# Kernel optimization log

Hardware: AMD Instinct MI355X
Metric: run time of the kernel (lower is better)

## Reference

```python
import jax, jax.numpy as jnp
import numpy as np

N_USERS, N_ITEMS, D, K, B = 1000000, 500000, 64, 256, 16384


def _l2norm(x, axis=1, eps=1e-12):
    n = jnp.sqrt(jnp.sum(x * x, axis=axis, keepdims=True))
    return x / jnp.maximum(n, eps)


def _sinkhorn(out):
    # out: [B, K]; 3 Sinkhorn-Knopp iterations on Q = exp(out/0.05).T
    Q = jnp.exp(out / 0.05).T            # [K, B]
    Kd, Bd = Q.shape
    Q = Q / jnp.sum(Q)
    for _ in range(3):
        Q = Q / (jnp.sum(Q, axis=1, keepdims=True) * Kd)
        Q = Q / (jnp.sum(Q, axis=0, keepdims=True) * Bd)
    return (Q * Bd).T                    # [B, K]


def _ce(q, code, gamma):
    return -jnp.mean(jnp.sum(q * jax.nn.log_softmax(code / gamma, axis=1), axis=1))


def setup_inputs() -> dict:
    key = jax.random.key(0)
    ks = jax.random.split(key, 8)
    return {
        "user_embeddings": jax.random.normal(ks[0], (N_USERS, D), jnp.float32),
        "id_embeddings": jax.random.normal(ks[1], (N_ITEMS, D), jnp.float32),
        "image_embeddings": jax.random.normal(ks[2], (N_ITEMS, D), jnp.float32),
        "text_embeddings": jax.random.normal(ks[3], (N_ITEMS, D), jnp.float32),
        "users": jax.random.randint(ks[4], (B,), 0, N_USERS, jnp.int32),
        "items": jax.random.randint(ks[5], (B,), 0, N_ITEMS, jnp.int32),
        "feat2code_w": jax.random.normal(ks[6], (K, D), jnp.float32),
        "ii2code_w": jax.random.normal(ks[7], (K, D), jnp.float32),
        "gamma": jnp.asarray(0.5, jnp.float32),
    }


def reference(user_embeddings, id_embeddings, image_embeddings, text_embeddings,
              users, items, feat2code_w, ii2code_w, gamma):
    # in-place clamp / weight renorm in torch happen under no_grad: value changes,
    # gradient wrt the parameter is identity -> straight-through here.
    g = gamma + jax.lax.stop_gradient(jnp.clip(gamma, 0.01, 0.99) - gamma)
    w_feat = feat2code_w + jax.lax.stop_gradient(_l2norm(feat2code_w) - feat2code_w)
    w_ii = ii2code_w + jax.lax.stop_gradient(_l2norm(ii2code_w) - ii2code_w)

    u = _l2norm(user_embeddings[users])     # [B, D]
    i_id = _l2norm(id_embeddings[items])
    i_im = _l2norm(image_embeddings[items])
    i_tx = _l2norm(text_embeddings[items])

    code_user = u @ w_feat.T                # [B, K]
    code_id = i_id @ w_feat.T
    code_id_ii = i_id @ w_ii.T
    code_image_ii = i_im @ w_ii.T
    code_text_ii = i_tx @ w_ii.T

    q_id = jax.lax.stop_gradient(_sinkhorn(code_id))
    q_user = jax.lax.stop_gradient(_sinkhorn(code_user))
    q_id_ii = jax.lax.stop_gradient(_sinkhorn(code_id_ii))
    q_image_ii = jax.lax.stop_gradient(_sinkhorn(code_image_ii))
    q_text_ii = jax.lax.stop_gradient(_sinkhorn(code_text_ii))

    loss = _ce(q_user, code_id, g) + _ce(q_id, code_user, g)
    align = (_ce(q_id_ii, code_image_ii, g) + _ce(q_id_ii, code_text_ii, g)
             + _ce(q_image_ii, code_id_ii, g) + _ce(q_image_ii, code_text_ii, g)
             + _ce(q_text_ii, code_id_ii, g) + _ce(q_text_ii, code_image_ii, g))
    return loss / 2 + align / 6
```

## Files before the change

kernel.cpp:

```cpp
#include <hip/hip_runtime.h>
#include <hip/hip_bf16.h>
#include <math.h>

#define BATCH 16384
#define DIM   64
#define KCODE 256

typedef unsigned short ushort_t;
typedef __attribute__((ext_vector_type(8))) short bf16x8;
typedef __attribute__((ext_vector_type(4))) float f32x4;

#define MFMA16 __builtin_amdgcn_mfma_f32_16x16x32_bf16

static __device__ __forceinline__ float ss4(float4 a) {
    return a.x*a.x + a.y*a.y + a.z*a.z + a.w*a.w;
}
static __device__ __forceinline__ short f2bs(float f) {
    unsigned u = __float_as_uint(f);
    u += 0x7FFFu + ((u >> 16) & 1u);
    return (short)(u >> 16);
}
static __device__ __forceinline__ bf16x8 pack8(float4 a, float4 b, float s) {
    bf16x8 r;
    r[0]=f2bs(a.x*s); r[1]=f2bs(a.y*s); r[2]=f2bs(a.z*s); r[3]=f2bs(a.w*s);
    r[4]=f2bs(b.x*s); r[5]=f2bs(b.y*s); r[6]=f2bs(b.z*s); r[7]=f2bs(b.w*s);
    return r;
}

__global__ __launch_bounds__(256) void k1_prep_gemm_cs1(
    const float* __restrict__ ue, const float* __restrict__ ie,
    const float* __restrict__ me, const float* __restrict__ te,
    const int* __restrict__ users, const int* __restrict__ items,
    const float* __restrict__ wfeat, const float* __restrict__ wii,
    ushort_t* __restrict__ An, ushort_t* __restrict__ Wn,
    float* __restrict__ cs1)
{
    const int m  = blockIdx.y;
    const int bx = blockIdx.x;
    const int t  = threadIdx.x;
    const int aset = (m==0) ? 0 : (m<3) ? 1 : (m==3) ? 2 : 3;
    const int wset = (m<2) ? 0 : 1;
    const float* asrc = (aset==0)?ue:(aset==1)?ie:(aset==2)?me:te;
    const int*  idxv = (m==0)?users:items;
    const float* wsrc = (wset==0)?wfeat:wii;
    const bool store_w = ((m==0 || m==2) && bx==0);
    const bool store_a = (m != 2);

    __shared__ short Wl[16384];
    __shared__ short Al[4096];
    __shared__ float redA[4][64];
    __shared__ float csl[256];

    {
        const float4* wp = (const float4*)(wsrc + t*DIM);
        float4 q[16]; float ss = 0.f;
        #pragma unroll
        for (int i=0;i<16;++i){ q[i]=wp[i]; ss += ss4(q[i]); }
        const float inv = 1.0f / fmaxf(sqrtf(ss), 1e-12f);
        const int kt = t>>4, lr = t&15;
        #pragma unroll
        for (int kk=0;kk<2;++kk)
            #pragma unroll
            for (int fs=0;fs<4;++fs){
                const int qi = kk*8 + fs*2;
                bf16x8 pk = pack8(q[qi], q[qi+1], inv);
                const int cid = (kt*2+kk)*64 + fs*16 + lr;
                *(bf16x8*)&Wl[cid*8] = pk;
                if (store_w)
                    *(bf16x8*)(Wn + ((size_t)wset*KCODE + t)*DIM + kk*32 + fs*8) = pk;
            }
    }

    const int rb = t&63, seg = t>>6;
    const int gidx = idxv[bx*64 + rb];
    const float4* ap = (const float4*)(asrc + (size_t)gidx*DIM + seg*16);
    float4 a0=ap[0], a1=ap[1], a2=ap[2], a3=ap[3];
    redA[seg][rb] = ss4(a0)+ss4(a1)+ss4(a2)+ss4(a3);
    csl[t] = 0.f;
    __syncthreads();

    {
        const float tot = redA[0][rb]+redA[1][rb]+redA[2][rb]+redA[3][rb];
        const float inv = 1.0f/fmaxf(sqrtf(tot),1e-12f);
        bf16x8 c0 = pack8(a0, a1, inv);
        bf16x8 c1 = pack8(a2, a3, inv);
        const int kk = seg>>1, fs0 = (seg&1)*2;
        const int base = ((rb>>4)*2 + kk)*64;
        *(bf16x8*)&Al[(base + fs0*16     + (rb&15))*8] = c0;
        *(bf16x8*)&Al[(base + (fs0+1)*16 + (rb&15))*8] = c1;
        if (store_a) {
            ushort_t* dst = An + ((size_t)aset*BATCH + bx*64 + rb)*DIM + seg*16;
            *(bf16x8*)dst       = c0;
            *(bf16x8*)(dst + 8) = c1;
        }
    }
    __syncthreads();

    const int w = t>>6, lane = t&63;
    bf16x8 af0 = *(bf16x8*)&Al[((w*2+0)*64 + lane)*8];
    bf16x8 af1 = *(bf16x8*)&Al[((w*2+1)*64 + lane)*8];
    #pragma unroll 4
    for (int kt=0; kt<16; ++kt){
        bf16x8 wf0 = *(bf16x8*)&Wl[((kt*2+0)*64 + lane)*8];
        bf16x8 wf1 = *(bf16x8*)&Wl[((kt*2+1)*64 + lane)*8];
        f32x4 acc = {0.f,0.f,0.f,0.f};
        acc = MFMA16(af0, wf0, acc, 0,0,0);
        acc = MFMA16(af1, wf1, acc, 0,0,0);
        float es = __expf(20.f*acc[0]) + __expf(20.f*acc[1])
                 + __expf(20.f*acc[2]) + __expf(20.f*acc[3]);
        atomicAdd(&csl[kt*16 + (lane&15)], es);
    }
    __syncthreads();
    atomicAdd(&cs1[m*KCODE + t], csl[t]);
}

__global__ __launch_bounds__(256) void k_pass(
    const ushort_t* __restrict__ An, const ushort_t* __restrict__ Wn,
    const float* __restrict__ cs_prev, float* __restrict__ cs_next)
{
    const int m = blockIdx.y;
    const int aset = (m==0)?0:(m<3)?1:(m==3)?2:3;
    const int wset = (m<2)?0:1;
    const int t = threadIdx.x, lane = t&63, w = t>>6;

    __shared__ short Wl[16384];
    __shared__ float csl[256];

    #pragma unroll
    for (int c8=0;c8<8;++c8){
        const int cid = c8*256 + t;
        const int kt = cid>>7, kk=(cid>>6)&1, ln=cid&63;
        const ushort_t* src = Wn + ((size_t)wset*KCODE + kt*16 + (ln&15))*DIM
                                 + kk*32 + (ln>>4)*8;
        *(bf16x8*)&Wl[cid*8] = *(const bf16x8*)src;
    }
    csl[t] = 0.f;
    float ar[16];
    #pragma unroll
    for (int kt=0;kt<16;++kt)
        ar[kt] = __builtin_amdgcn_rcpf(256.0f * cs_prev[m*KCODE + kt*16 + (lane&15)]);
    __syncthreads();

    float csp[16];
    #pragma unroll
    for (int kt=0;kt<16;++kt) csp[kt]=0.f;

    for (int rt = blockIdx.x*4 + w; rt < BATCH/16; rt += gridDim.x*4){
        const int r0 = rt*16;
        const ushort_t* ab = An + ((size_t)aset*BATCH + r0 + (lane&15))*DIM + (lane>>4)*8;
        bf16x8 af0 = *(const bf16x8*)ab;
        bf16x8 af1 = *(const bf16x8*)(ab + 32);
        float ev[16][4];
        float sp0=0.f, sp1=0.f, sp2=0.f, sp3=0.f;
        #pragma unroll
        for (int kt=0;kt<16;++kt){
            bf16x8 wf0 = *(bf16x8*)&Wl[((kt*2+0)*64+lane)*8];
            bf16x8 wf1 = *(bf16x8*)&Wl[((kt*2+1)*64+lane)*8];
            f32x4 acc = {0.f,0.f,0.f,0.f};
            acc = MFMA16(af0, wf0, acc, 0,0,0);
            acc = MFMA16(af1, wf1, acc, 0,0,0);
            ev[kt][0]=__expf(20.f*acc[0]); ev[kt][1]=__expf(20.f*acc[1]);
            ev[kt][2]=__expf(20.f*acc[2]); ev[kt][3]=__expf(20.f*acc[3]);
            sp0 = fmaf(ar[kt], ev[kt][0], sp0);
            sp1 = fmaf(ar[kt], ev[kt][1], sp1);
            sp2 = fmaf(ar[kt], ev[kt][2], sp2);
            sp3 = fmaf(ar[kt], ev[kt][3], sp3);
        }
        #pragma unroll
        for (int off=8; off>=1; off>>=1){
            sp0 += __shfl_xor(sp0, off, 64);
            sp1 += __shfl_xor(sp1, off, 64);
            sp2 += __shfl_xor(sp2, off, 64);
            sp3 += __shfl_xor(sp3, off, 64);
        }
        const float b0 = __builtin_amdgcn_rcpf(16384.f*sp0);
        const float b1 = __builtin_amdgcn_rcpf(16384.f*sp1);
        const float b2 = __builtin_amdgcn_rcpf(16384.f*sp2);
        const float b3 = __builtin_amdgcn_rcpf(16384.f*sp3);
        #pragma unroll
        for (int kt=0;kt<16;++kt)
            csp[kt] += ev[kt][0]*b0 + ev[kt][1]*b1 + ev[kt][2]*b2 + ev[kt][3]*b3;
    }
    #pragma unroll
    for (int kt=0;kt<16;++kt)
        atomicAdd(&csl[kt*16 + (lane&15)], csp[kt]);
    __syncthreads();
    atomicAdd(&cs_next[m*KCODE + t], csl[t]);
}

__global__ __launch_bounds__(256) void k_ce(
    const ushort_t* __restrict__ An, const ushort_t* __restrict__ Wn,
    const float* __restrict__ cs3, const float* __restrict__ gamma_p,
    float* __restrict__ out)
{
    const int t = threadIdx.x, lane = t&63, w = t>>6;
    __shared__ short Wl[32768];
    __shared__ float al[1280];

    #pragma unroll
    for (int c16=0;c16<16;++c16){
        const int cid = c16*256 + t;
        const int ws = cid>>11, rem = cid&2047;
        const int kt = rem>>7, kk=(rem>>6)&1, ln=rem&63;
        const ushort_t* src = Wn + ((size_t)ws*KCODE + kt*16 + (ln&15))*DIM
                                 + kk*32 + (ln>>4)*8;
        *(bf16x8*)&Wl[cid*8] = *(const bf16x8*)src;
    }
    #pragma unroll
    for (int mm=0;mm<5;++mm)
        al[mm*256+t] = __builtin_amdgcn_rcpf(256.0f * cs3[mm*KCODE + t]);
    const float g = fminf(fmaxf(gamma_p[0], 0.01f), 0.99f);
    const float invg = 1.0f/g;
    __syncthreads();

    float wacc = 0.f;
    for (int rt = blockIdx.x*4 + w; rt < BATCH/16; rt += gridDim.x*4){
        const int r0 = rt*16;
        bf16x8 af[4][2];
        #pragma unroll
        for (int s=0;s<4;++s){
            const ushort_t* ab = An + ((size_t)s*BATCH + r0 + (lane&15))*DIM + (lane>>4)*8;
            af[s][0] = *(const bf16x8*)ab;
            af[s][1] = *(const bf16x8*)(ab + 32);
        }
        float S[5][4], L[5][4], DP[5][4];
        #pragma unroll
        for (int mm=0;mm<5;++mm)
            #pragma unroll
            for (int r=0;r<4;++r){ S[mm][r]=0.f; L[mm][r]=0.f; DP[mm][r]=0.f; }

        #pragma unroll 2
        for (int kt=0;kt<16;++kt){
            bf16x8 wf[2][2];
            #pragma unroll
            for (int ws=0;ws<2;++ws){
                wf[ws][0] = *(bf16x8*)&Wl[((ws*2048) + (kt*2+0)*64 + lane)*8];
                wf[ws][1] = *(bf16x8*)&Wl[((ws*2048) + (kt*2+1)*64 + lane)*8];
            }
            const f32x4 Z = {0.f,0.f,0.f,0.f};
            f32x4 c[5];
            c[0] = MFMA16(af[0][0], wf[0][0], Z, 0,0,0);
            c[0] = MFMA16(af[0][1], wf[0][1], c[0], 0,0,0);
            c[1] = MFMA16(af[1][0], wf[0][0], Z, 0,0,0);
            c[1] = MFMA16(af[1][1], wf[0][1], c[1], 0,0,0);
            c[2] = MFMA16(af[1][0], wf[1][0], Z, 0,0,0);
            c[2] = MFMA16(af[1][1], wf[1][1], c[2], 0,0,0);
            c[3] = MFMA16(af[2][0], wf[1][0], Z, 0,0,0);
            c[3] = MFMA16(af[2][1], wf[1][1], c[3], 0,0,0);
            c[4] = MFMA16(af[3][0], wf[1][0], Z, 0,0,0);
            c[4] = MFMA16(af[3][1], wf[1][1], c[4], 0,0,0);

            float am[5];
            #pragma unroll
            for (int mm=0;mm<5;++mm) am[mm] = al[mm*256 + kt*16 + (lane&15)];

            float fm[5][4];
            #pragma unroll
            for (int mm=0;mm<5;++mm)
                #pragma unroll
                for (int r=0;r<4;++r){
                    const float cv = c[mm][r];
                    const float f = am[mm] * __expf(20.f*cv);
                    fm[mm][r] = f;
                    S[mm][r] += f;
                    L[mm][r] += __expf(invg*cv);
                }
            #pragma unroll
            for (int r=0;r<4;++r){
                DP[0][r] = fmaf(fm[0][r], c[1][r], DP[0][r]);
                DP[1][r] = fmaf(fm[1][r], c[0][r], DP[1][r]);
                const float c34 = c[3][r]+c[4][r];
                const float c24 = c[2][r]+c[4][r];
                const float c23 = c[2][r]+c[3][r];
                DP[2][r] = fmaf(fm[2][r], c34, DP[2][r]);
                DP[3][r] = fmaf(fm[3][r], c24, DP[3][r]);
                DP[4][r] = fmaf(fm[4][r], c23, DP[4][r]);
            }
        }
        #pragma unroll
        for (int off=8; off>=1; off>>=1)
            #pragma unroll
            for (int mm=0;mm<5;++mm)
                #pragma unroll
                for (int r=0;r<4;++r){
                    S[mm][r]  += __shfl_xor(S[mm][r],  off, 64);
                    L[mm][r]  += __shfl_xor(L[mm][r],  off, 64);
                    DP[mm][r] += __shfl_xor(DP[mm][r], off, 64);
                }
        #pragma unroll
        for (int r=0;r<4;++r){
            const float u =
                0.5f*(DP[0][r]*__builtin_amdgcn_rcpf(S[0][r])
                    + DP[1][r]*__builtin_amdgcn_rcpf(S[1][r]))
              + (1.f/6.f)*(DP[2][r]*__builtin_amdgcn_rcpf(S[2][r])
                         + DP[3][r]*__builtin_amdgcn_rcpf(S[3][r])
                         + DP[4][r]*__builtin_amdgcn_rcpf(S[4][r]));
            const float Lr =
                0.5f*(__logf(L[0][r]) + __logf(L[1][r]))
              + (1.f/3.f)*(__logf(L[2][r]) + __logf(L[3][r]) + __logf(L[4][r]));
            wacc += Lr - invg*u;
        }
    }
    wacc += __shfl_xor(wacc, 16, 64);
    wacc += __shfl_xor(wacc, 32, 64);
    if (lane == 0) atomicAdd(out, wacc * (1.0f/16384.0f));
}

extern "C" void kernel_launch(void* const* d_in, const int* in_sizes, int n_in,
                              void* d_out, int out_size, void* d_ws, size_t ws_size,
                              hipStream_t stream)
{
    const float* ue    = (const float*)d_in[0];
    const float* ie    = (const float*)d_in[1];
    const float* me    = (const float*)d_in[2];
    const float* te    = (const float*)d_in[3];
    const int*   users = (const int*)d_in[4];
    const int*   items = (const int*)d_in[5];
    const float* wfeat = (const float*)d_in[6];
    const float* wii   = (const float*)d_in[7];
    const float* gamma = (const float*)d_in[8];
    float* out = (float*)d_out;

    ushort_t* An = (ushort_t*)d_ws;
    ushort_t* Wn = An + (size_t)4*BATCH*DIM;
    float* cs  = (float*)(Wn + 2*KCODE*DIM);
    float* cs1 = cs;
    float* cs2 = cs + 1280;
    float* cs3 = cs + 2560;

    hipMemsetAsync(out, 0, sizeof(float), stream);
    hipMemsetAsync(cs, 0, 3*1280*sizeof(float), stream);

    k1_prep_gemm_cs1<<<dim3(256,5), 256, 0, stream>>>(
        ue, ie, me, te, users, items, wfeat, wii, An, Wn, cs1);
    k_pass<<<dim3(128,5), 256, 0, stream>>>(An, Wn, cs1, cs2);
    k_pass<<<dim3(128,5), 256, 0, stream>>>(An, Wn, cs2, cs3);
    k_ce<<<256, 256, 0, stream>>>(An, Wn, cs3, gamma, out);
}
```

Measured before the change: 146.6 us.

## Merge prep, Sinkhorn passes and CE into one cooperative persistent kernel

Replaces the four separate launches and two memsets with a single cooperative kernel. It uses grid-wide syncs between the normalization/bf16 packing stage, the three Sinkhorn column-sum passes and the cross-entropy stage. The goal is to remove launch gaps and memset overhead, and to load both normalized weight sets into LDS once per block for all stages. In exchange the first Sinkhorn pass no longer runs in the prep stage, so it re-reads An from global memory. Each tile now also does per-tile shared atomics, and the grid size is capped by occupancy (74KB LDS per block).

```diff
diff --git a/kernel.cpp b/kernel.cpp
--- a/kernel.cpp
+++ b/kernel.cpp
@@ -1,6 +1,8 @@
 #include <hip/hip_runtime.h>
-#include <hip/hip_bf16.h>
+#include <hip/hip_cooperative_groups.h>
 #include <math.h>
+
+namespace cg = cooperative_groups;
 
 #define BATCH 16384
 #define DIM   64
@@ -27,194 +29,183 @@
     return r;
 }
 
-__global__ __launch_bounds__(256) void k1_prep_gemm_cs1(
+template<bool FIRST>
+static __device__ __forceinline__ void sink_pass(
+    const ushort_t* __restrict__ An, const short* __restrict__ Wl,
+    const float* __restrict__ al, float* __restrict__ csl,
+    int wid, int lane, int nW)
+{
+    for (int u = wid; u < 5120; u += nW) {
+        const int m = u >> 10, rt = u & 1023;
+        const int aset = (m==0) ? 0 : (m<3) ? 1 : (m==3) ? 2 : 3;
+        const int wset = (m<2) ? 0 : 1;
+        const ushort_t* ab = An + ((size_t)aset*BATCH + rt*16 + (lane&15))*DIM + (lane>>4)*8;
+        bf16x8 af0 = *(const bf16x8*)ab;
+        bf16x8 af1 = *(const bf16x8*)(ab + 32);
+        float csp[16];
+        if (FIRST) {
+            #pragma unroll
+            for (int kt=0;kt<16;++kt){
+                bf16x8 wf0 = *(const bf16x8*)&Wl[((wset*2048)+(kt*2+0)*64+lane)*8];
+                bf16x8 wf1 = *(const bf16x8*)&Wl[((wset*2048)+(kt*2+1)*64+lane)*8];
+                f32x4 acc = {0.f,0.f,0.f,0.f};
+                acc = MFMA16(af0, wf0, acc, 0,0,0);
+                acc = MFMA16(af1, wf1, acc, 0,0,0);
+                csp[kt] = __expf(20.f*acc[0]) + __expf(20.f*acc[1])
+                        + __expf(20.f*acc[2]) + __expf(20.f*acc[3]);
+            }
+        } else {
+            float ev[16][4];
+            float sp0=0.f, sp1=0.f, sp2=0.f, sp3=0.f;
+            #pragma unroll
+            for (int kt=0;kt<16;++kt){
+                bf16x8 wf0 = *(const bf16x8*)&Wl[((wset*2048)+(kt*2+0)*64+lane)*8];
+                bf16x8 wf1 = *(const bf16x8*)&Wl[((wset*2048)+(kt*2+1)*64+lane)*8];
+                f32x4 acc = {0.f,0.f,0.f,0.f};
+                acc = MFMA16(af0, wf0, acc, 0,0,0);
+                acc = MFMA16(af1, wf1, acc, 0,0,0);
+                ev[kt][0]=__expf(20.f*acc[0]); ev[kt][1]=__expf(20.f*acc[1]);
+                ev[kt][2]=__expf(20.f*acc[2]); ev[kt][3]=__expf(20.f*acc[3]);
+                const float a = al[m*KCODE + kt*16 + (lane&15)];
+                sp0 = fmaf(a, ev[kt][0], sp0);
+                sp1 = fmaf(a, ev[kt][1], sp1);
+                sp2 = fmaf(a, ev[kt][2], sp2);
+                sp3 = fmaf(a, ev[kt][3], sp3);
+            }
+            #pragma unroll
+            for (int off=8; off>=1; off>>=1){
+                sp0 += __shfl_xor(sp0, off, 64);
+                sp1 += __shfl_xor(sp1, off, 64);
+                sp2 += __shfl_xor(sp2, off, 64);
+                sp3 += __shfl_xor(sp3, off, 64);
+            }
+            const float b0 = __builtin_amdgcn_rcpf(16384.f*sp0);
+            const float b1 = __builtin_amdgcn_rcpf(16384.f*sp1);
+            const float b2 = __builtin_amdgcn_rcpf(16384.f*sp2);
+            const float b3 = __builtin_amdgcn_rcpf(16384.f*sp3);
+            #pragma unroll
+            for (int kt=0;kt<16;++kt)
+                csp[kt] = ev[kt][0]*b0 + ev[kt][1]*b1 + ev[kt][2]*b2 + ev[kt][3]*b3;
+        }
+        #pragma unroll
+        for (int kt=0;kt<16;++kt){
+            float v = csp[kt];
+            v += __shfl_xor(v, 16, 64);
+            v += __shfl_xor(v, 32, 64);
+            if (lane < 16) atomicAdd(&csl[m*KCODE + kt*16 + lane], v);
+        }
+    }
+}
+
+__global__ __launch_bounds__(256, 2) void cla_mega(
     const float* __restrict__ ue, const float* __restrict__ ie,
     const float* __restrict__ me, const float* __restrict__ te,
     const int* __restrict__ users, const int* __restrict__ items,
     const float* __restrict__ wfeat, const float* __restrict__ wii,
     ushort_t* __restrict__ An, ushort_t* __restrict__ Wn,
-    float* __restrict__ cs1)
-{
-    const int m  = blockIdx.y;
-    const int bx = blockIdx.x;
-    const int t  = threadIdx.x;
-    const int aset = (m==0) ? 0 : (m<3) ? 1 : (m==3) ? 2 : 3;
-    const int wset = (m<2) ? 0 : 1;
-    const float* asrc = (aset==0)?ue:(aset==1)?ie:(aset==2)?me:te;
-    const int*  idxv = (m==0)?users:items;
-    const float* wsrc = (wset==0)?wfeat:wii;
-    const bool store_w = ((m==0 || m==2) && bx==0);
-    const bool store_a = (m != 2);
-
-    __shared__ short Wl[16384];
-    __shared__ short Al[4096];
-    __shared__ float redA[4][64];
-    __shared__ float csl[256];
-
-    {
-        const float4* wp = (const float4*)(wsrc + t*DIM);
-        float4 q[16]; float ss = 0.f;
-        #pragma unroll
-        for (int i=0;i<16;++i){ q[i]=wp[i]; ss += ss4(q[i]); }
-        const float inv = 1.0f / fmaxf(sqrtf(ss), 1e-12f);
-        const int kt = t>>4, lr = t&15;
-        #pragma unroll
-        for (int kk=0;kk<2;++kk)
-            #pragma unroll
-            for (int fs=0;fs<4;++fs){
-                const int qi = kk*8 + fs*2;
-                bf16x8 pk = pack8(q[qi], q[qi+1], inv);
-                const int cid = (kt*2+kk)*64 + fs*16 + lr;
-                *(bf16x8*)&Wl[cid*8] = pk;
-                if (store_w)
-                    *(bf16x8*)(Wn + ((size_t)wset*KCODE + t)*DIM + kk*32 + fs*8) = pk;
-            }
-    }
-
-    const int rb = t&63, seg = t>>6;
-    const int gidx = idxv[bx*64 + rb];
-    const float4* ap = (const float4*)(asrc + (size_t)gidx*DIM + seg*16);
-    float4 a0=ap[0], a1=ap[1], a2=ap[2], a3=ap[3];
-    redA[seg][rb] = ss4(a0)+ss4(a1)+ss4(a2)+ss4(a3);
-    csl[t] = 0.f;
-    __syncthreads();
-
-    {
-        const float tot = redA[0][rb]+redA[1][rb]+redA[2][rb]+redA[3][rb];
-        const float inv = 1.0f/fmaxf(sqrtf(tot),1e-12f);
-        bf16x8 c0 = pack8(a0, a1, inv);
-        bf16x8 c1 = pack8(a2, a3, inv);
-        const int kk = seg>>1, fs0 = (seg&1)*2;
-        const int base = ((rb>>4)*2 + kk)*64;
-        *(bf16x8*)&Al[(base + fs0*16     + (rb&15))*8] = c0;
-        *(bf16x8*)&Al[(base + (fs0+1)*16 + (rb&15))*8] = c1;
-        if (store_a) {
-            ushort_t* dst = An + ((size_t)aset*BATCH + bx*64 + rb)*DIM + seg*16;
-            *(bf16x8*)dst       = c0;
-            *(bf16x8*)(dst + 8) = c1;
-        }
-    }
-    __syncthreads();
-
-    const int w = t>>6, lane = t&63;
-    bf16x8 af0 = *(bf16x8*)&Al[((w*2+0)*64 + lane)*8];
-    bf16x8 af1 = *(bf16x8*)&Al[((w*2+1)*64 + lane)*8];
-    #pragma unroll 4
-    for (int kt=0; kt<16; ++kt){
-        bf16x8 wf0 = *(bf16x8*)&Wl[((kt*2+0)*64 + lane)*8];
-        bf16x8 wf1 = *(bf16x8*)&Wl[((kt*2+1)*64 + lane)*8];
-        f32x4 acc = {0.f,0.f,0.f,0.f};
-        acc = MFMA16(af0, wf0, acc, 0,0,0);
-        acc = MFMA16(af1, wf1, acc, 0,0,0);
-        float es = __expf(20.f*acc[0]) + __expf(20.f*acc[1])
-                 + __expf(20.f*acc[2]) + __expf(20.f*acc[3]);
-        atomicAdd(&csl[kt*16 + (lane&15)], es);
-    }
-    __syncthreads();
-    atomicAdd(&cs1[m*KCODE + t], csl[t]);
-}
-
-__global__ __launch_bounds__(256) void k_pass(
-    const ushort_t* __restrict__ An, const ushort_t* __restrict__ Wn,
-    const float* __restrict__ cs_prev, float* __restrict__ cs_next)
-{
-    const int m = blockIdx.y;
-    const int aset = (m==0)?0:(m<3)?1:(m==3)?2:3;
-    const int wset = (m<2)?0:1;
-    const int t = threadIdx.x, lane = t&63, w = t>>6;
-
-    __shared__ short Wl[16384];
-    __shared__ float csl[256];
-
-    #pragma unroll
-    for (int c8=0;c8<8;++c8){
-        const int cid = c8*256 + t;
-        const int kt = cid>>7, kk=(cid>>6)&1, ln=cid&63;
-        const ushort_t* src = Wn + ((size_t)wset*KCODE + kt*16 + (ln&15))*DIM
-                                 + kk*32 + (ln>>4)*8;
-        *(bf16x8*)&Wl[cid*8] = *(const bf16x8*)src;
-    }
-    csl[t] = 0.f;
-    float ar[16];
-    #pragma unroll
-    for (int kt=0;kt<16;++kt)
-        ar[kt] = __builtin_amdgcn_rcpf(256.0f * cs_prev[m*KCODE + kt*16 + (lane&15)]);
-    __syncthreads();
-
-    float csp[16];
-    #pragma unroll
-    for (int kt=0;kt<16;++kt) csp[kt]=0.f;
-
-    for (int rt = blockIdx.x*4 + w; rt < BATCH/16; rt += gridDim.x*4){
-        const int r0 = rt*16;
-        const ushort_t* ab = An + ((size_t)aset*BATCH + r0 + (lane&15))*DIM + (lane>>4)*8;
-        bf16x8 af0 = *(const bf16x8*)ab;
-        bf16x8 af1 = *(const bf16x8*)(ab + 32);
-        float ev[16][4];
-        float sp0=0.f, sp1=0.f, sp2=0.f, sp3=0.f;
-        #pragma unroll
-        for (int kt=0;kt<16;++kt){
-            bf16x8 wf0 = *(bf16x8*)&Wl[((kt*2+0)*64+lane)*8];
-            bf16x8 wf1 = *(bf16x8*)&Wl[((kt*2+1)*64+lane)*8];
-            f32x4 acc = {0.f,0.f,0.f,0.f};
-            acc = MFMA16(af0, wf0, acc, 0,0,0);
-            acc = MFMA16(af1, wf1, acc, 0,0,0);
-            ev[kt][0]=__expf(20.f*acc[0]); ev[kt][1]=__expf(20.f*acc[1]);
-            ev[kt][2]=__expf(20.f*acc[2]); ev[kt][3]=__expf(20.f*acc[3]);
-            sp0 = fmaf(ar[kt], ev[kt][0], sp0);
-            sp1 = fmaf(ar[kt], ev[kt][1], sp1);
-            sp2 = fmaf(ar[kt], ev[kt][2], sp2);
-            sp3 = fmaf(ar[kt], ev[kt][3], sp3);
-        }
-        #pragma unroll
-        for (int off=8; off>=1; off>>=1){
-            sp0 += __shfl_xor(sp0, off, 64);
-            sp1 += __shfl_xor(sp1, off, 64);
-            sp2 += __shfl_xor(sp2, off, 64);
-            sp3 += __shfl_xor(sp3, off, 64);
-        }
-        const float b0 = __builtin_amdgcn_rcpf(16384.f*sp0);
-        const float b1 = __builtin_amdgcn_rcpf(16384.f*sp1);
-        const float b2 = __builtin_amdgcn_rcpf(16384.f*sp2);
-        const float b3 = __builtin_amdgcn_rcpf(16384.f*sp3);
-        #pragma unroll
-        for (int kt=0;kt<16;++kt)
-            csp[kt] += ev[kt][0]*b0 + ev[kt][1]*b1 + ev[kt][2]*b2 + ev[kt][3]*b3;
-    }
-    #pragma unroll
-    for (int kt=0;kt<16;++kt)
-        atomicAdd(&csl[kt*16 + (lane&15)], csp[kt]);
-    __syncthreads();
-    atomicAdd(&cs_next[m*KCODE + t], csl[t]);
-}
-
-__global__ __launch_bounds__(256) void k_ce(
-    const ushort_t* __restrict__ An, const ushort_t* __restrict__ Wn,
-    const float* __restrict__ cs3, const float* __restrict__ gamma_p,
+    float* __restrict__ cs, const float* __restrict__ gamma_p,
     float* __restrict__ out)
 {
-    const int t = threadIdx.x, lane = t&63, w = t>>6;
+    cg::grid_group gg = cg::this_grid();
+    const int t = threadIdx.x, lane = t & 63;
+    const int g = blockIdx.x*256 + t;
+    const int wid = (blockIdx.x*256 + t) >> 6;
+    const int nT = gridDim.x << 8;
+    const int nW = gridDim.x << 2;
+
     __shared__ short Wl[32768];
     __shared__ float al[1280];
-
-    #pragma unroll
-    for (int c16=0;c16<16;++c16){
-        const int cid = c16*256 + t;
-        const int ws = cid>>11, rem = cid&2047;
-        const int kt = rem>>7, kk=(rem>>6)&1, ln=rem&63;
-        const ushort_t* src = Wn + ((size_t)ws*KCODE + kt*16 + (ln&15))*DIM
-                                 + kk*32 + (ln>>4)*8;
-        *(bf16x8*)&Wl[cid*8] = *(const bf16x8*)src;
-    }
-    #pragma unroll
-    for (int mm=0;mm<5;++mm)
-        al[mm*256+t] = __builtin_amdgcn_rcpf(256.0f * cs3[mm*KCODE + t]);
-    const float g = fminf(fmaxf(gamma_p[0], 0.01f), 0.99f);
-    const float invg = 1.0f/g;
-    __syncthreads();
-
+    __shared__ float csl[1280];
+
+    for (int i = g; i < 3840; i += nT) cs[i] = 0.f;
+    if (g == 0) out[0] = 0.f;
+
+    for (int h = g; h < 2*4*BATCH; h += nT) {
+        const int row = h >> 1, half = h & 1;
+        const int set = row >> 14, r = row & (BATCH-1);
+        const float* src; int idx;
+        if (set == 0)      { src = ue; idx = users[r]; }
+        else if (set == 1) { src = ie; idx = items[r]; }
+        else if (set == 2) { src = me; idx = items[r]; }
+        else               { src = te; idx = items[r]; }
+        const float4* p = (const float4*)(src + (size_t)idx*DIM + half*32);
+        float4 q[8]; float ss = 0.f;
+        #pragma unroll
+        for (int i2=0;i2<8;++i2){ q[i2]=p[i2]; ss += ss4(q[i2]); }
+        ss += __shfl_xor(ss, 1, 64);
+        const float inv = 1.0f / fmaxf(sqrtf(ss), 1e-12f);
+        ushort_t* dst = An + ((size_t)set*BATCH + r)*DIM + half*32;
+        #pragma unroll
+        for (int j=0;j<4;++j)
+            *(bf16x8*)(dst + j*8) = pack8(q[2*j], q[2*j+1], inv);
+    }
+    for (int h = g; h < 2*2*KCODE; h += nT) {
+        const int wrow = h >> 1, half = h & 1;
+        const int wset = wrow >> 8, wr = wrow & 255;
+        const float* src = (wset ? wii : wfeat) + (size_t)wr*DIM + half*32;
+        const float4* p = (const float4*)src;
+        float4 q[8]; float ss = 0.f;
+        #pragma unroll
+        for (int i2=0;i2<8;++i2){ q[i2]=p[i2]; ss += ss4(q[i2]); }
+        ss += __shfl_xor(ss, 1, 64);
+        const float inv = 1.0f / fmaxf(sqrtf(ss), 1e-12f);
+        ushort_t* dst = Wn + ((size_t)wset*KCODE + wr)*DIM + half*32;
+        #pragma unroll
+        for (int j=0;j<4;++j)
+            *(bf16x8*)(dst + j*8) = pack8(q[2*j], q[2*j+1], inv);
+    }
+    gg.sync();
+
+    for (int cid = t; cid < 4096; cid += 256) {
+        const int ws2 = cid >> 11, rem = cid & 2047;
+        const int kt = rem >> 7, kk = (rem >> 6) & 1, ln = rem & 63;
+        const ushort_t* s2 = Wn + ((size_t)ws2*KCODE + kt*16 + (ln&15))*DIM
+                                + kk*32 + (ln>>4)*8;
+        *(bf16x8*)&Wl[cid*8] = *(const bf16x8*)s2;
+    }
+    #pragma unroll
+    for (int j=0;j<5;++j) csl[j*256+t] = 0.f;
+    __syncthreads();
+
+    sink_pass<true>(An, Wl, al, csl, wid, lane, nW);
+    __syncthreads();
+    #pragma unroll
+    for (int j=0;j<5;++j) atomicAdd(&cs[j*256+t], csl[j*256+t]);
+    gg.sync();
+
+    #pragma unroll
+    for (int j=0;j<5;++j){
+        al[j*256+t]  = __builtin_amdgcn_rcpf(256.0f * cs[j*256+t]);
+        csl[j*256+t] = 0.f;
+    }
+    __syncthreads();
+    sink_pass<false>(An, Wl, al, csl, wid, lane, nW);
+    __syncthreads();
+    #pragma unroll
+    for (int j=0;j<5;++j) atomicAdd(&cs[1280 + j*256+t], csl[j*256+t]);
+    gg.sync();
+
+    #pragma unroll
+    for (int j=0;j<5;++j){
+        al[j*256+t]  = __builtin_amdgcn_rcpf(256.0f * cs[1280 + j*256+t]);
+        csl[j*256+t] = 0.f;
+    }
+    __syncthreads();
+    sink_pass<false>(An, Wl, al, csl, wid, lane, nW);
+    __syncthreads();
+    #pragma unroll
+    for (int j=0;j<5;++j) atomicAdd(&cs[2560 + j*256+t], csl[j*256+t]);
+    gg.sync();
+
+    #pragma unroll
+    for (int j=0;j<5;++j)
+        al[j*256+t] = __builtin_amdgcn_rcpf(256.0f * cs[2560 + j*256+t]);
+    __syncthreads();
+
+    const float gam = fminf(fmaxf(gamma_p[0], 0.01f), 0.99f);
+    const float invg = 1.0f / gam;
     float wacc = 0.f;
-    for (int rt = blockIdx.x*4 + w; rt < BATCH/16; rt += gridDim.x*4){
+    for (int rt = wid; rt < 1024; rt += nW) {
         const int r0 = rt*16;
         bf16x8 af[4][2];
         #pragma unroll
@@ -233,9 +224,9 @@
         for (int kt=0;kt<16;++kt){
             bf16x8 wf[2][2];
             #pragma unroll
-            for (int ws=0;ws<2;++ws){
-                wf[ws][0] = *(bf16x8*)&Wl[((ws*2048) + (kt*2+0)*64 + lane)*8];
-                wf[ws][1] = *(bf16x8*)&Wl[((ws*2048) + (kt*2+1)*64 + lane)*8];
+            for (int ws2=0;ws2<2;++ws2){
+                wf[ws2][0] = *(const bf16x8*)&Wl[((ws2*2048)+(kt*2+0)*64+lane)*8];
+                wf[ws2][1] = *(const bf16x8*)&Wl[((ws2*2048)+(kt*2+1)*64+lane)*8];
             }
             const f32x4 Z = {0.f,0.f,0.f,0.f};
             f32x4 c[5];
@@ -252,7 +243,7 @@
 
             float am[5];
             #pragma unroll
-            for (int mm=0;mm<5;++mm) am[mm] = al[mm*256 + kt*16 + (lane&15)];
+            for (int mm=0;mm<5;++mm) am[mm] = al[mm*KCODE + kt*16 + (lane&15)];
 
             float fm[5][4];
             #pragma unroll
@@ -323,17 +314,16 @@
 
     ushort_t* An = (ushort_t*)d_ws;
     ushort_t* Wn = An + (size_t)4*BATCH*DIM;
-    float* cs  = (float*)(Wn + 2*KCODE*DIM);
-    float* cs1 = cs;
-    float* cs2 = cs + 1280;
-    float* cs3 = cs + 2560;
-
-    hipMemsetAsync(out, 0, sizeof(float), stream);
-    hipMemsetAsync(cs, 0, 3*1280*sizeof(float), stream);
-
-    k1_prep_gemm_cs1<<<dim3(256,5), 256, 0, stream>>>(
-        ue, ie, me, te, users, items, wfeat, wii, An, Wn, cs1);
-    k_pass<<<dim3(128,5), 256, 0, stream>>>(An, Wn, cs1, cs2);
-    k_pass<<<dim3(128,5), 256, 0, stream>>>(An, Wn, cs2, cs3);
-    k_ce<<<256, 256, 0, stream>>>(An, Wn, cs3, gamma, out);
-}
+    float* cs = (float*)(Wn + 2*KCODE*DIM);
+
+    int maxPerCU = 0;
+    hipOccupancyMaxActiveBlocksPerMultiprocessor(&maxPerCU, cla_mega, 256, 0);
+    int nBlk = (maxPerCU > 0 ? maxPerCU : 1) * 256;
+    if (nBlk > 512) nBlk = 512;
+
+    void* args[] = { (void*)&ue, (void*)&ie, (void*)&me, (void*)&te,
+                     (void*)&users, (void*)&items, (void*)&wfeat, (void*)&wii,
+                     (void*)&An, (void*)&Wn, (void*)&cs, (void*)&gamma,
+                     (void*)&out };
+    hipLaunchCooperativeKernel(cla_mega, dim3(nBlk), dim3(256), args, 0, stream);
+}
```

Measured after the change: 222.3 us. +51.6%, slower.
